# Kernel optimization log

Measured on AMD Instinct MI355X. Metric: run time of the kernel, lower is better.

## Reference

```python
import jax, jax.numpy as jnp
import numpy as np

N = 100000
E = 1600000
D = 64  # in = hidden = out channels


def setup_inputs() -> dict:
    key = jax.random.key(0)
    ks = jax.random.split(key, 6)
    x = jax.random.normal(ks[0], (N, D), dtype=jnp.float32)
    edge_index = jax.random.randint(ks[1], (2, E), 0, N, dtype=jnp.int64)
    # bias-free linear weights, torch Linear layout [out, in]
    s = 1.0 / np.sqrt(D)
    W0 = jax.random.uniform(ks[2], (D, D), jnp.float32, -s, s)
    W1 = jax.random.uniform(ks[3], (D, D), jnp.float32, -s, s)
    Wm = jax.random.uniform(ks[4], (D, D), jnp.float32, -s, s)
    eps0 = jnp.zeros((), jnp.float32)  # train_eps=True, init 0.0
    eps1 = jnp.zeros((), jnp.float32)
    return {"x": x, "edge_index": edge_index, "W0": W0, "eps0": eps0,
            "W1": W1, "eps1": eps1, "Wm": Wm}


def reference(x, edge_index, W0, eps0, W1, eps1, Wm):
    n = x.shape[0]
    src, dst = edge_index[0], edge_index[1]

    def gin_conv(h, W, eps):
        # sparse adjacency sum-aggregation: out[i] = sum_{j->i} h[j]
        agg = jax.ops.segment_sum(h[src], dst, num_segments=n)
        # eps-scaled self-loop + bias-free linear
        return (agg + (1.0 + eps) * h) @ W.T

    h1 = jax.nn.relu(gin_conv(x, W0, eps0))   # xs[0], [N, D]
    h2 = jax.nn.relu(gin_conv(h1, W1, eps1))  # xs[1], [N, D]
    return (h1 @ Wm.T + h2) / 2.0
```

## Files before the change

kernel.cpp:

```cpp
#include <hip/hip_runtime.h>
#include <hip/hip_fp16.h>


__global__ __launch_bounds__(256) void zero_int_kernel(int* __restrict__ p, int n)
{
    int i = blockIdx.x * blockDim.x + threadIdx.x;
    int stride = gridDim.x * blockDim.x;
    for (; i < n; i += stride) p[i] = 0;
}

__global__ __launch_bounds__(256) void hist_rank_kernel(
    const int* __restrict__ dst, int* __restrict__ deg,
    int* __restrict__ rank, int E)
{
    int base = (blockIdx.x * blockDim.x + threadIdx.x) * 16;
    if (base + 15 < E) {
        int4 a = *(const int4*)&dst[base];
        int4 b = *(const int4*)&dst[base + 4];
        int4 c = *(const int4*)&dst[base + 8];
        int4 d = *(const int4*)&dst[base + 12];
        int r0 = atomicAdd(&deg[a.x], 1);
        int r1 = atomicAdd(&deg[a.y], 1);
        int r2 = atomicAdd(&deg[a.z], 1);
        int r3 = atomicAdd(&deg[a.w], 1);
        int r4 = atomicAdd(&deg[b.x], 1);
        int r5 = atomicAdd(&deg[b.y], 1);
        int r6 = atomicAdd(&deg[b.z], 1);
        int r7 = atomicAdd(&deg[b.w], 1);
        int r8 = atomicAdd(&deg[c.x], 1);
        int r9 = atomicAdd(&deg[c.y], 1);
        int rA = atomicAdd(&deg[c.z], 1);
        int rB = atomicAdd(&deg[c.w], 1);
        int rC = atomicAdd(&deg[d.x], 1);
        int rD = atomicAdd(&deg[d.y], 1);
        int rE = atomicAdd(&deg[d.z], 1);
        int rF = atomicAdd(&deg[d.w], 1);
        *(int4*)&rank[base]      = make_int4(r0, r1, r2, r3);
        *(int4*)&rank[base + 4]  = make_int4(r4, r5, r6, r7);
        *(int4*)&rank[base + 8]  = make_int4(r8, r9, rA, rB);
        *(int4*)&rank[base + 12] = make_int4(rC, rD, rE, rF);
    } else {
        for (int e = base; e < E; ++e) rank[e] = atomicAdd(&deg[dst[e]], 1);
    }
}

__global__ __launch_bounds__(256) void hist_kernel(
    const int* __restrict__ dst, int* __restrict__ deg, int E)
{
    int e4 = (blockIdx.x * blockDim.x + threadIdx.x) * 4;
    if (e4 + 3 < E) {
        int4 d = *(const int4*)&dst[e4];
        atomicAdd(&deg[d.x], 1);
        atomicAdd(&deg[d.y], 1);
        atomicAdd(&deg[d.z], 1);
        atomicAdd(&deg[d.w], 1);
    } else {
        for (int e = e4; e < E; ++e) atomicAdd(&deg[dst[e]], 1);
    }
}

__global__ __launch_bounds__(256) void scanA_kernel(
    const int* __restrict__ deg, int* __restrict__ off,
    int* __restrict__ bsum, int n)
{
    __shared__ int tmp[256];
    int t = threadIdx.x;
    int base = blockIdx.x * 1024 + t * 4;
    int v0 = 0, v1 = 0, v2 = 0, v3 = 0;
    if (base + 3 < n) {
        int4 q = *(const int4*)&deg[base];
        v0 = q.x; v1 = q.y; v2 = q.z; v3 = q.w;
    } else {
        if (base + 0 < n) v0 = deg[base + 0];
        if (base + 1 < n) v1 = deg[base + 1];
        if (base + 2 < n) v2 = deg[base + 2];
    }
    int tot = v0 + v1 + v2 + v3;
    tmp[t] = tot;
    __syncthreads();
    for (int d = 1; d < 256; d <<= 1) {
        int x = (t >= d) ? tmp[t - d] : 0;
        __syncthreads();
        tmp[t] += x;
        __syncthreads();
    }
    int incl = tmp[t];
    int p = incl - tot;
    if (base + 0 < n) off[base + 0] = p;
    if (base + 1 < n) off[base + 1] = p + v0;
    if (base + 2 < n) off[base + 2] = p + v0 + v1;
    if (base + 3 < n) off[base + 3] = p + v0 + v1 + v2;
    if (t == 255) bsum[blockIdx.x] = incl;
}

__global__ __launch_bounds__(256) void scanB_kernel(int* __restrict__ bsum, int nb)
{
    __shared__ int tmp[256];
    int t = threadIdx.x;
    int v = (t < nb) ? bsum[t] : 0;
    tmp[t] = v;
    __syncthreads();
    for (int d = 1; d < 256; d <<= 1) {
        int x = (t >= d) ? tmp[t - d] : 0;
        __syncthreads();
        tmp[t] += x;
        __syncthreads();
    }
    if (t < nb) bsum[t] = tmp[t] - v;
}

__global__ __launch_bounds__(256) void scanC_kernel(
    int* __restrict__ off, int* __restrict__ cursor,
    const int* __restrict__ bsum, int n, int E)
{
    int t = threadIdx.x;
    int add = bsum[blockIdx.x];
    int base = blockIdx.x * 1024 + t * 4;
#pragma unroll
    for (int q = 0; q < 4; ++q) {
        int idx = base + q;
        if (idx < n) {
            int v = off[idx] + add;
            off[idx] = v;
            if (cursor) cursor[idx] = v;
        }
    }
    if (blockIdx.x == 0 && t == 0) off[n] = E;
}

__global__ __launch_bounds__(256) void fill_rank_kernel(
    const int* __restrict__ src, const int* __restrict__ dst,
    const int* __restrict__ rank, const int* __restrict__ off,
    int* __restrict__ bucket, int E)
{
    int base = (blockIdx.x * blockDim.x + threadIdx.x) * 8;
    if (base + 7 < E) {
        int4 d0 = *(const int4*)&dst[base];
        int4 d1 = *(const int4*)&dst[base + 4];
        int4 r0 = *(const int4*)&rank[base];
        int4 r1 = *(const int4*)&rank[base + 4];
        int4 s0 = *(const int4*)&src[base];
        int4 s1 = *(const int4*)&src[base + 4];
        bucket[off[d0.x] + r0.x] = s0.x;
        bucket[off[d0.y] + r0.y] = s0.y;
        bucket[off[d0.z] + r0.z] = s0.z;
        bucket[off[d0.w] + r0.w] = s0.w;
        bucket[off[d1.x] + r1.x] = s1.x;
        bucket[off[d1.y] + r1.y] = s1.y;
        bucket[off[d1.z] + r1.z] = s1.z;
        bucket[off[d1.w] + r1.w] = s1.w;
    } else {
        for (int e = base; e < E; ++e) bucket[off[dst[e]] + rank[e]] = src[e];
    }
}

__global__ __launch_bounds__(256) void fill_kernel(
    const int* __restrict__ src, const int* __restrict__ dst,
    int* __restrict__ cursor, int* __restrict__ bucket, int E)
{
    int e = blockIdx.x * blockDim.x + threadIdx.x;
    if (e < E) {
        int d = dst[e];
        int p = atomicAdd(&cursor[d], 1);
        bucket[p] = src[e];
    }
}

__global__ __launch_bounds__(256) void f32_to_f16_kernel(
    const float* __restrict__ in, __half* __restrict__ out, int total4)
{
    int i = blockIdx.x * blockDim.x + threadIdx.x;
    int stride = gridDim.x * blockDim.x;
    const float4* in4 = (const float4*)in;
    uint2* out4 = (uint2*)out;
    for (; i < total4; i += stride) {
        float4 v = in4[i];
        __half2 a = __floats2half2_rn(v.x, v.y);
        __half2 b = __floats2half2_rn(v.z, v.w);
        uint2 u;
        u.x = __builtin_bit_cast(unsigned int, a);
        u.y = __builtin_bit_cast(unsigned int, b);
        out4[i] = u;
    }
}

#define WPB 8

__device__ __forceinline__ __half2 bc_h2(unsigned int u)
{
    return __builtin_bit_cast(__half2, u);
}
__device__ __forceinline__ unsigned int bc_u(__half2 h)
{
    return __builtin_bit_cast(unsigned int, h);
}

#if __has_builtin(__builtin_amdgcn_fdot2)
typedef _Float16 half2_v __attribute__((ext_vector_type(2)));
__device__ __forceinline__ float fdot2(unsigned int a, unsigned int b, float c)
{
    return __builtin_amdgcn_fdot2(__builtin_bit_cast(half2_v, a),
                                  __builtin_bit_cast(half2_v, b), c, false);
}
#else
__device__ __forceinline__ float fdot2(unsigned int a, unsigned int b, float c)
{
    float2 af = __half22float2(bc_h2(a));
    float2 bf = __half22float2(bc_h2(b));
    return fmaf(af.x, bf.x, fmaf(af.y, bf.y, c));
}
#endif

__device__ __forceinline__ void xreduce4(__half2& a0, __half2& a1,
                                         __half2& a2, __half2& a3)
{
#pragma unroll
    for (int mask = 8; mask <= 32; mask <<= 1) {
        a0 = __hadd2(a0, bc_h2((unsigned int)__shfl_xor((int)bc_u(a0), mask, 64)));
        a1 = __hadd2(a1, bc_h2((unsigned int)__shfl_xor((int)bc_u(a1), mask, 64)));
        a2 = __hadd2(a2, bc_h2((unsigned int)__shfl_xor((int)bc_u(a2), mask, 64)));
        a3 = __hadd2(a3, bc_h2((unsigned int)__shfl_xor((int)bc_u(a3), mask, 64)));
    }
}

__device__ __forceinline__ void gather8(
    const __half* __restrict__ hh, const int* __restrict__ bucket,
    int beg, int end, int g, int l8,
    __half2& a0, __half2& a1, __half2& a2, __half2& a3)
{
    int j = beg;
    for (; j + 16 <= end; j += 16) {
        int sa = bucket[j + g];
        int sb = bucket[j + 8 + g];
        uint4 va = *(const uint4*)&hh[(size_t)sa * 64 + l8 * 8];
        uint4 vb = *(const uint4*)&hh[(size_t)sb * 64 + l8 * 8];
        a0 = __hadd2(__hadd2(a0, bc_h2(va.x)), bc_h2(vb.x));
        a1 = __hadd2(__hadd2(a1, bc_h2(va.y)), bc_h2(vb.y));
        a2 = __hadd2(__hadd2(a2, bc_h2(va.z)), bc_h2(vb.z));
        a3 = __hadd2(__hadd2(a3, bc_h2(va.w)), bc_h2(vb.w));
    }
    if (j + 8 <= end) {
        int sa = bucket[j + g];
        uint4 va = *(const uint4*)&hh[(size_t)sa * 64 + l8 * 8];
        a0 = __hadd2(a0, bc_h2(va.x));
        a1 = __hadd2(a1, bc_h2(va.y));
        a2 = __hadd2(a2, bc_h2(va.z));
        a3 = __hadd2(a3, bc_h2(va.w));
        j += 8;
    }
    if (j < end) {
        int jj = j + g;
        int sc = bucket[(jj < end) ? jj : (end - 1)];
        __half2 m2 = __float2half2_rn((jj < end) ? 1.0f : 0.0f);
        uint4 vc = *(const uint4*)&hh[(size_t)sc * 64 + l8 * 8];
        a0 = __hfma2(bc_h2(vc.x), m2, a0);
        a1 = __hfma2(bc_h2(vc.y), m2, a1);
        a2 = __hfma2(bc_h2(vc.z), m2, a2);
        a3 = __hfma2(bc_h2(vc.w), m2, a3);
    }
}


__global__ __launch_bounds__(512) void fused_gin_h_kernel(
    const __half* __restrict__ hh, const int* __restrict__ off,
    const int* __restrict__ bucket, const float* __restrict__ W,
    const float* __restrict__ eps, __half* __restrict__ outh, int n)
{
    __shared__ __half WhS[4096];
    __shared__ __half rowh[WPB][64];
    int tid = threadIdx.x;
    for (int idx = tid; idx < 4096; idx += 512) {
        int row = idx >> 6, col = idx & 63;
        WhS[(col >> 3) * 512 + row * 8 + (col & 7)] = __float2half(W[idx]);
    }
    __syncthreads();
    float s = 1.0f + eps[0];
    __half2 s2 = __float2half2_rn(s);
    int lane = tid & 63;
    int w = tid >> 6;
    int l8 = lane & 7;
    int g = lane >> 3;
    int wavesTotal = gridDim.x * WPB;
    const uint4* Wh4 = (const uint4*)WhS;
    for (int i = blockIdx.x * WPB + w; i < n; i += wavesTotal) {
        int2 be = *(const int2*)&off[i];
        int beg = __builtin_amdgcn_readfirstlane(be.x);
        int end = __builtin_amdgcn_readfirstlane(be.y);
        __half2 a0 = bc_h2(0u), a1 = bc_h2(0u), a2 = bc_h2(0u), a3 = bc_h2(0u);
        gather8(hh, bucket, beg, end, g, l8, a0, a1, a2, a3);
        xreduce4(a0, a1, a2, a3);
        if (g == 0) {
            uint4 sv = *(const uint4*)&hh[(size_t)i * 64 + l8 * 8];
            a0 = __hfma2(bc_h2(sv.x), s2, a0);
            a1 = __hfma2(bc_h2(sv.y), s2, a1);
            a2 = __hfma2(bc_h2(sv.z), s2, a2);
            a3 = __hfma2(bc_h2(sv.w), s2, a3);
            uint4 st;
            st.x = bc_u(a0); st.y = bc_u(a1); st.z = bc_u(a2); st.w = bc_u(a3);
            *(uint4*)&rowh[w][l8 * 8] = st;
        }
        __builtin_amdgcn_wave_barrier();
        float o = 0.f;
#pragma unroll
        for (int k4 = 0; k4 < 8; ++k4) {
            uint4 wv = Wh4[k4 * 64 + lane];
            uint4 rv = *(const uint4*)&rowh[w][k4 * 8];
            o = fdot2(wv.x, rv.x, o);
            o = fdot2(wv.y, rv.y, o);
            o = fdot2(wv.z, rv.z, o);
            o = fdot2(wv.w, rv.w, o);
        }
        outh[(size_t)i * 64 + lane] = __float2half(fmaxf(o, 0.f));
        __builtin_amdgcn_wave_barrier();
    }
}

__global__ __launch_bounds__(512) void fused_final_h_kernel(
    const __half* __restrict__ hh1, const int* __restrict__ off,
    const int* __restrict__ bucket, const float* __restrict__ W1,
    const float* __restrict__ Wm, const float* __restrict__ eps,
    float* __restrict__ out, int n)
{
    __shared__ __half W1hS[4096];
    __shared__ __half WmhS[4096];
    __shared__ __half rowh[WPB][64];
    __shared__ __half selfh[WPB][64];
    int tid = threadIdx.x;
    for (int idx = tid; idx < 4096; idx += 512) {
        int row = idx >> 6, col = idx & 63;
        int li = (col >> 3) * 512 + row * 8 + (col & 7);
        W1hS[li] = __float2half(W1[idx]);
        WmhS[li] = __float2half(Wm[idx]);
    }
    __syncthreads();
    float s = 1.0f + eps[0];
    __half2 s2 = __float2half2_rn(s);
    int lane = tid & 63;
    int w = tid >> 6;
    int l8 = lane & 7;
    int g = lane >> 3;
    int wavesTotal = gridDim.x * WPB;
    const uint4* W1h4 = (const uint4*)W1hS;
    const uint4* Wmh4 = (const uint4*)WmhS;
    for (int i = blockIdx.x * WPB + w; i < n; i += wavesTotal) {
        int2 be = *(const int2*)&off[i];
        int beg = __builtin_amdgcn_readfirstlane(be.x);
        int end = __builtin_amdgcn_readfirstlane(be.y);
        __half2 a0 = bc_h2(0u), a1 = bc_h2(0u), a2 = bc_h2(0u), a3 = bc_h2(0u);
        gather8(hh1, bucket, beg, end, g, l8, a0, a1, a2, a3);
        xreduce4(a0, a1, a2, a3);
        if (g == 0) {
            uint4 sv = *(const uint4*)&hh1[(size_t)i * 64 + l8 * 8];
            *(uint4*)&selfh[w][l8 * 8] = sv;
            a0 = __hfma2(bc_h2(sv.x), s2, a0);
            a1 = __hfma2(bc_h2(sv.y), s2, a1);
            a2 = __hfma2(bc_h2(sv.z), s2, a2);
            a3 = __hfma2(bc_h2(sv.w), s2, a3);
            uint4 st;
            st.x = bc_u(a0); st.y = bc_u(a1); st.z = bc_u(a2); st.w = bc_u(a3);
            *(uint4*)&rowh[w][l8 * 8] = st;
        }
        __builtin_amdgcn_wave_barrier();
        float o1 = 0.f, o2 = 0.f;
#pragma unroll
        for (int k4 = 0; k4 < 8; ++k4) {
            uint4 wv1 = W1h4[k4 * 64 + lane];
            uint4 wv2 = Wmh4[k4 * 64 + lane];
            uint4 rv  = *(const uint4*)&rowh[w][k4 * 8];
            uint4 sv  = *(const uint4*)&selfh[w][k4 * 8];
            o1 = fdot2(wv1.x, rv.x, o1);
            o1 = fdot2(wv1.y, rv.y, o1);
            o1 = fdot2(wv1.z, rv.z, o1);
            o1 = fdot2(wv1.w, rv.w, o1);
            o2 = fdot2(wv2.x, sv.x, o2);
            o2 = fdot2(wv2.y, sv.y, o2);
            o2 = fdot2(wv2.z, sv.z, o2);
            o2 = fdot2(wv2.w, sv.w, o2);
        }
        out[(size_t)i * 64 + lane] = (fmaxf(o1, 0.f) + o2) * 0.5f;
        __builtin_amdgcn_wave_barrier();
    }
}

__device__ __forceinline__ float dot4(float4 a, float4 b)
{
    return a.x * b.x + a.y * b.y + a.z * b.z + a.w * b.w;
}

__device__ __forceinline__ float4 gather_row_f32(
    const float* __restrict__ h, const int* __restrict__ bucket,
    int beg, int end, int g, int l16, float4 acc4)
{
    int j = beg;
    for (; j + 8 <= end; j += 8) {
        int sa = bucket[j + g];
        int sb = bucket[j + 4 + g];
        float4 va = *(const float4*)&h[(size_t)sa * 64 + l16 * 4];
        float4 vb = *(const float4*)&h[(size_t)sb * 64 + l16 * 4];
        acc4.x += va.x + vb.x;
        acc4.y += va.y + vb.y;
        acc4.z += va.z + vb.z;
        acc4.w += va.w + vb.w;
    }
    if (j + 4 <= end) {
        int sa = bucket[j + g];
        float4 va = *(const float4*)&h[(size_t)sa * 64 + l16 * 4];
        acc4.x += va.x; acc4.y += va.y; acc4.z += va.z; acc4.w += va.w;
        j += 4;
    }
    if (j < end) {
        int jj = j + g;
        int sc = bucket[(jj < end) ? jj : (end - 1)];
        float m = (jj < end) ? 1.0f : 0.0f;
        float4 vc = *(const float4*)&h[(size_t)sc * 64 + l16 * 4];
        acc4.x = fmaf(vc.x, m, acc4.x);
        acc4.y = fmaf(vc.y, m, acc4.y);
        acc4.z = fmaf(vc.z, m, acc4.z);
        acc4.w = fmaf(vc.w, m, acc4.w);
    }
    return acc4;
}

__global__ __launch_bounds__(512) void fused_gin_kernel(
    const float* __restrict__ h, const int* __restrict__ off,
    const int* __restrict__ bucket, const float* __restrict__ W,
    const float* __restrict__ eps, float* __restrict__ out, int n)
{
    __shared__ float Ws[64][68];
    __shared__ float P[WPB][4][64];
    __shared__ float rowbuf[WPB][64];
    int tid = threadIdx.x;
    for (int idx = tid; idx < 4096; idx += 512) Ws[idx >> 6][idx & 63] = W[idx];
    __syncthreads();
    float s = 1.0f + eps[0];
    int lane = tid & 63;
    int w = tid >> 6;
    int l16 = lane & 15;
    int g = lane >> 4;
    int wavesTotal = gridDim.x * WPB;
    for (int i = blockIdx.x * WPB + w; i < n; i += wavesTotal) {
        float4 init = make_float4(0.f, 0.f, 0.f, 0.f);
        if (g == 0) {
            float4 self4 = *(const float4*)&h[(size_t)i * 64 + l16 * 4];
            init = make_float4(s * self4.x, s * self4.y, s * self4.z, s * self4.w);
        }
        int2 be = *(const int2*)&off[i];
        int beg = __builtin_amdgcn_readfirstlane(be.x);
        int end = __builtin_amdgcn_readfirstlane(be.y);
        float4 acc4 = gather_row_f32(h, bucket, beg, end, g, l16, init);
        *(float4*)&P[w][g][l16 * 4] = acc4;
        __builtin_amdgcn_wave_barrier();
        float r0 = P[w][0][lane], r1 = P[w][1][lane];
        float r2 = P[w][2][lane], r3 = P[w][3][lane];
        rowbuf[w][lane] = (r0 + r1) + (r2 + r3);
        __builtin_amdgcn_wave_barrier();
        const float4* wrow = (const float4*)&Ws[lane][0];
        const float4* rrow = (const float4*)&rowbuf[w][0];
        float o = 0.f;
#pragma unroll
        for (int k4 = 0; k4 < 16; ++k4) o += dot4(wrow[k4], rrow[k4]);
        out[(size_t)i * 64 + lane] = fmaxf(o, 0.f);
        __builtin_amdgcn_wave_barrier();
    }
}

__global__ __launch_bounds__(512) void fused_final_csr_kernel(
    const float* __restrict__ h1, const int* __restrict__ off,
    const int* __restrict__ bucket, const float* __restrict__ W1,
    const float* __restrict__ Wm, const float* __restrict__ eps,
    float* __restrict__ out, int n)
{
    __shared__ float W1s[64][68];
    __shared__ float Wms[64][68];
    __shared__ float P[WPB][4][64];
    __shared__ float rowbuf[WPB][64];
    __shared__ float selfbuf[WPB][64];
    int tid = threadIdx.x;
    for (int idx = tid; idx < 4096; idx += 512) {
        W1s[idx >> 6][idx & 63] = W1[idx];
        Wms[idx >> 6][idx & 63] = Wm[idx];
    }
    __syncthreads();
    float s = 1.0f + eps[0];
    int lane = tid & 63;
    int w = tid >> 6;
    int l16 = lane & 15;
    int g = lane >> 4;
    int wavesTotal = gridDim.x * WPB;
    for (int i = blockIdx.x * WPB + w; i < n; i += wavesTotal) {
        float4 init = make_float4(0.f, 0.f, 0.f, 0.f);
        if (g == 0) {
            float4 self4 = *(const float4*)&h1[(size_t)i * 64 + l16 * 4];
            *(float4*)&selfbuf[w][l16 * 4] = self4;
            init = make_float4(s * self4.x, s * self4.y, s * self4.z, s * self4.w);
        }
        int2 be = *(const int2*)&off[i];
        int beg = __builtin_amdgcn_readfirstlane(be.x);
        int end = __builtin_amdgcn_readfirstlane(be.y);
        float4 acc4 = gather_row_f32(h1, bucket, beg, end, g, l16, init);
        *(float4*)&P[w][g][l16 * 4] = acc4;
        __builtin_amdgcn_wave_barrier();
        float r0 = P[w][0][lane], r1 = P[w][1][lane];
        float r2 = P[w][2][lane], r3 = P[w][3][lane];
        rowbuf[w][lane] = (r0 + r1) + (r2 + r3);
        __builtin_amdgcn_wave_barrier();
        const float4* w1row = (const float4*)&W1s[lane][0];
        const float4* wmrow = (const float4*)&Wms[lane][0];
        const float4* rrow  = (const float4*)&rowbuf[w][0];
        const float4* srow  = (const float4*)&selfbuf[w][0];
        float o1 = 0.f, o2 = 0.f;
#pragma unroll
        for (int k4 = 0; k4 < 16; ++k4) {
            o1 += dot4(w1row[k4], rrow[k4]);
            o2 += dot4(wmrow[k4], srow[k4]);
        }
        out[(size_t)i * 64 + lane] = (fmaxf(o1, 0.f) + o2) * 0.5f;
        __builtin_amdgcn_wave_barrier();
    }
}

__global__ __launch_bounds__(256) void init_scale_kernel(
    const float* __restrict__ h, const float* __restrict__ eps,
    float* __restrict__ agg, int total4)
{
    float s = 1.0f + eps[0];
    int i = blockIdx.x * blockDim.x + threadIdx.x;
    int stride = gridDim.x * blockDim.x;
    const float4* h4 = (const float4*)h;
    float4* a4 = (float4*)agg;
    for (; i < total4; i += stride) {
        float4 v = h4[i];
        v.x *= s; v.y *= s; v.z *= s; v.w *= s;
        a4[i] = v;
    }
}

__global__ __launch_bounds__(256) void scatter_kernel(
    const float* __restrict__ h, const int* __restrict__ src,
    const int* __restrict__ dst, float* __restrict__ agg, int E)
{
    int lane = threadIdx.x & 63;
    int e = blockIdx.x * 4 + (threadIdx.x >> 6);
    if (e >= E) return;
    int s = src[e];
    int d = dst[e];
    atomicAdd(&agg[(size_t)d * 64 + lane], h[(size_t)s * 64 + lane]);
}

__global__ __launch_bounds__(256) void gemm_relu_kernel(
    const float* __restrict__ A, const float* __restrict__ W,
    float* __restrict__ out, int n)
{
    __shared__ float Wt[64][65];
    __shared__ float rowbuf[4][64];
    int tid = threadIdx.x;
    for (int i = tid; i < 4096; i += 256) Wt[i & 63][i >> 6] = W[i];
    __syncthreads();
    int lane = tid & 63;
    int w = tid >> 6;
    int wavesTotal = gridDim.x * 4;
    for (int i = blockIdx.x * 4 + w; i < n; i += wavesTotal) {
        rowbuf[w][lane] = A[(size_t)i * 64 + lane];
        __builtin_amdgcn_wave_barrier();
        float o = 0.f;
#pragma unroll
        for (int k = 0; k < 64; ++k) o += rowbuf[w][k] * Wt[k][lane];
        out[(size_t)i * 64 + lane] = fmaxf(o, 0.f);
        __builtin_amdgcn_wave_barrier();
    }
}

__global__ __launch_bounds__(256) void final_kernel(
    const float* __restrict__ Agg, const float* __restrict__ H1,
    const float* __restrict__ W1, const float* __restrict__ Wm,
    float* __restrict__ out, int n)
{
    __shared__ float W1t[64][65];
    __shared__ float Wmt[64][65];
    __shared__ float rowbuf[4][64];
    __shared__ float selfbuf[4][64];
    int tid = threadIdx.x;
    for (int i = tid; i < 4096; i += 256) {
        W1t[i & 63][i >> 6] = W1[i];
        Wmt[i & 63][i >> 6] = Wm[i];
    }
    __syncthreads();
    int lane = tid & 63;
    int w = tid >> 6;
    int wavesTotal = gridDim.x * 4;
    for (int i = blockIdx.x * 4 + w; i < n; i += wavesTotal) {
        rowbuf[w][lane] = Agg[(size_t)i * 64 + lane];
        selfbuf[w][lane] = H1[(size_t)i * 64 + lane];
        __builtin_amdgcn_wave_barrier();
        float o1 = 0.f, o2 = 0.f;
#pragma unroll
        for (int k = 0; k < 64; ++k) {
            o1 += rowbuf[w][k] * W1t[k][lane];
            o2 += selfbuf[w][k] * Wmt[k][lane];
        }
        out[(size_t)i * 64 + lane] = (fmaxf(o1, 0.f) + o2) * 0.5f;
        __builtin_amdgcn_wave_barrier();
    }
}

extern "C" void kernel_launch(void* const* d_in, const int* in_sizes, int n_in,
                              void* d_out, int out_size, void* d_ws, size_t ws_size,
                              hipStream_t stream)
{
    const float* x    = (const float*)d_in[0];
    const int*   ei   = (const int*)d_in[1];
    const float* W0   = (const float*)d_in[2];
    const float* eps0 = (const float*)d_in[3];
    const float* W1   = (const float*)d_in[4];
    const float* eps1 = (const float*)d_in[5];
    const float* Wm   = (const float*)d_in[6];
    float* out = (float*)d_out;

    int n = in_sizes[0] / 64;
    int E = in_sizes[1] / 2;
    const int* src = ei;
    const int* dst = ei + E;

    auto align1k = [](size_t v) { return (v + 1023) & ~(size_t)1023; };

    size_t hhx_off    = 0;
    size_t hh1_off    = align1k(hhx_off + (size_t)n * 64 * 2);
    size_t off_off    = align1k(hh1_off + (size_t)n * 64 * 2);
    size_t deg_off    = align1k(off_off + (size_t)(n + 1) * 4);
    size_t bsum_off   = align1k(deg_off + (size_t)n * 4);
    size_t bucket_off = align1k(bsum_off + 256 * 4);
    size_t rank_off   = align1k(bucket_off + (size_t)E * 4);
    size_t need_A2    = rank_off + (size_t)E * 4;

    size_t b_h1_off     = 0;
    size_t b_off_off    = align1k(b_h1_off + (size_t)n * 64 * 4);
    size_t b_deg_off    = align1k(b_off_off + (size_t)(n + 1) * 4);
    size_t b_cursor_off = align1k(b_deg_off + (size_t)n * 4);
    size_t b_bsum_off   = align1k(b_cursor_off + (size_t)n * 4);
    size_t b_bucket_off = align1k(b_bsum_off + 256 * 4);
    size_t need_B       = b_bucket_off + (size_t)E * 4;

    int nb = (n + 1023) / 1024;
    int e8Blocks  = (E + 2047) / 2048;
    int e16Blocks = (E + 4095) / 4096;
    int total4 = n * 16;

    if (ws_size >= need_A2) {
        __half* hhx  = (__half*)((char*)d_ws + hhx_off);
        __half* hh1  = (__half*)((char*)d_ws + hh1_off);
        int* off     = (int*)((char*)d_ws + off_off);
        int* deg     = (int*)((char*)d_ws + deg_off);
        int* bsum    = (int*)((char*)d_ws + bsum_off);
        int* bucket  = (int*)((char*)d_ws + bucket_off);
        int* rank    = (int*)((char*)d_ws + rank_off);

        zero_int_kernel<<<256, 256, 0, stream>>>(deg, n);
        f32_to_f16_kernel<<<2048, 256, 0, stream>>>(x, hhx, total4);
        hist_rank_kernel<<<e16Blocks, 256, 0, stream>>>(dst, deg, rank, E);
        scanA_kernel<<<nb, 256, 0, stream>>>(deg, off, bsum, n);
        scanB_kernel<<<1, 256, 0, stream>>>(bsum, nb);
        scanC_kernel<<<nb, 256, 0, stream>>>(off, (int*)nullptr, bsum, n, E);
        fill_rank_kernel<<<e8Blocks, 256, 0, stream>>>(src, dst, rank, off, bucket, E);

        fused_gin_h_kernel<<<1024, 512, 0, stream>>>(hhx, off, bucket, W0, eps0, hh1, n);
        fused_final_h_kernel<<<1024, 512, 0, stream>>>(hh1, off, bucket, W1, Wm, eps1, out, n);
    } else if (ws_size >= need_B) {
        float* h1    = (float*)((char*)d_ws + b_h1_off);
        int* off     = (int*)((char*)d_ws + b_off_off);
        int* deg     = (int*)((char*)d_ws + b_deg_off);
        int* cursor  = (int*)((char*)d_ws + b_cursor_off);
        int* bsum    = (int*)((char*)d_ws + b_bsum_off);
        int* bucket  = (int*)((char*)d_ws + b_bucket_off);

        zero_int_kernel<<<256, 256, 0, stream>>>(deg, n);
        hist_kernel<<<(E + 1023) / 1024, 256, 0, stream>>>(dst, deg, E);
        scanA_kernel<<<nb, 256, 0, stream>>>(deg, off, bsum, n);
        scanB_kernel<<<1, 256, 0, stream>>>(bsum, nb);
        scanC_kernel<<<nb, 256, 0, stream>>>(off, cursor, bsum, n, E);
        fill_kernel<<<(E + 255) / 256, 256, 0, stream>>>(src, dst, cursor, bucket, E);

        fused_gin_kernel<<<1024, 512, 0, stream>>>(x, off, bucket, W0, eps0, h1, n);
        fused_final_csr_kernel<<<768, 512, 0, stream>>>(h1, off, bucket, W1, Wm, eps1, out, n);
    } else {
        float* agg = (float*)d_ws;
        float* h1  = out;
        int scatterBlocks = (E + 3) / 4;

        init_scale_kernel<<<2048, 256, 0, stream>>>(x, eps0, agg, total4);
        scatter_kernel<<<scatterBlocks, 256, 0, stream>>>(x, src, dst, agg, E);
        gemm_relu_kernel<<<2048, 256, 0, stream>>>(agg, W0, h1, n);
        init_scale_kernel<<<2048, 256, 0, stream>>>(h1, eps1, agg, total4);
        scatter_kernel<<<scatterBlocks, 256, 0, stream>>>(h1, src, dst, agg, E);
        final_kernel<<<2048, 256, 0, stream>>>(agg, h1, W1, Wm, out, n);
    }
}
```

Measured before the change: 225.2 us.

## Process eight nodes per wave with per-octet gather and batched matvec

Each wave now handles eight destination nodes at once, with each 8-lane group gathering one node's neighbors. This replaces the old scheme where the whole wave split one node's edge list and then reduced across lanes with shuffles. The mat-vec step reuses each loaded weight vector across eight rows held in shared memory, and the grid drops to 784 blocks. The cost is lane divergence, since every group loops up to the wave's maximum degree with masked loads. Overshoot reads past the bucket array are covered by padding the workspace.

```diff
diff --git a/kernel.cpp b/kernel.cpp
--- a/kernel.cpp
+++ b/kernel.cpp
@@ -211,55 +211,6 @@
 }
 #endif
 
-__device__ __forceinline__ void xreduce4(__half2& a0, __half2& a1,
-                                         __half2& a2, __half2& a3)
-{
-#pragma unroll
-    for (int mask = 8; mask <= 32; mask <<= 1) {
-        a0 = __hadd2(a0, bc_h2((unsigned int)__shfl_xor((int)bc_u(a0), mask, 64)));
-        a1 = __hadd2(a1, bc_h2((unsigned int)__shfl_xor((int)bc_u(a1), mask, 64)));
-        a2 = __hadd2(a2, bc_h2((unsigned int)__shfl_xor((int)bc_u(a2), mask, 64)));
-        a3 = __hadd2(a3, bc_h2((unsigned int)__shfl_xor((int)bc_u(a3), mask, 64)));
-    }
-}
-
-__device__ __forceinline__ void gather8(
-    const __half* __restrict__ hh, const int* __restrict__ bucket,
-    int beg, int end, int g, int l8,
-    __half2& a0, __half2& a1, __half2& a2, __half2& a3)
-{
-    int j = beg;
-    for (; j + 16 <= end; j += 16) {
-        int sa = bucket[j + g];
-        int sb = bucket[j + 8 + g];
-        uint4 va = *(const uint4*)&hh[(size_t)sa * 64 + l8 * 8];
-        uint4 vb = *(const uint4*)&hh[(size_t)sb * 64 + l8 * 8];
-        a0 = __hadd2(__hadd2(a0, bc_h2(va.x)), bc_h2(vb.x));
-        a1 = __hadd2(__hadd2(a1, bc_h2(va.y)), bc_h2(vb.y));
-        a2 = __hadd2(__hadd2(a2, bc_h2(va.z)), bc_h2(vb.z));
-        a3 = __hadd2(__hadd2(a3, bc_h2(va.w)), bc_h2(vb.w));
-    }
-    if (j + 8 <= end) {
-        int sa = bucket[j + g];
-        uint4 va = *(const uint4*)&hh[(size_t)sa * 64 + l8 * 8];
-        a0 = __hadd2(a0, bc_h2(va.x));
-        a1 = __hadd2(a1, bc_h2(va.y));
-        a2 = __hadd2(a2, bc_h2(va.z));
-        a3 = __hadd2(a3, bc_h2(va.w));
-        j += 8;
-    }
-    if (j < end) {
-        int jj = j + g;
-        int sc = bucket[(jj < end) ? jj : (end - 1)];
-        __half2 m2 = __float2half2_rn((jj < end) ? 1.0f : 0.0f);
-        uint4 vc = *(const uint4*)&hh[(size_t)sc * 64 + l8 * 8];
-        a0 = __hfma2(bc_h2(vc.x), m2, a0);
-        a1 = __hfma2(bc_h2(vc.y), m2, a1);
-        a2 = __hfma2(bc_h2(vc.z), m2, a2);
-        a3 = __hfma2(bc_h2(vc.w), m2, a3);
-    }
-}
-
 
 __global__ __launch_bounds__(512) void fused_gin_h_kernel(
     const __half* __restrict__ hh, const int* __restrict__ off,
@@ -267,7 +218,7 @@
     const float* __restrict__ eps, __half* __restrict__ outh, int n)
 {
     __shared__ __half WhS[4096];
-    __shared__ __half rowh[WPB][64];
+    __shared__ __half rowh[WPB][8][64];
     int tid = threadIdx.x;
     for (int idx = tid; idx < 4096; idx += 512) {
         int row = idx >> 6, col = idx & 63;
@@ -276,41 +227,97 @@
     __syncthreads();
     float s = 1.0f + eps[0];
     __half2 s2 = __float2half2_rn(s);
+    const __half2 one2 = __float2half2_rn(1.0f);
+    const __half2 zero2 = __float2half2_rn(0.0f);
     int lane = tid & 63;
     int w = tid >> 6;
     int l8 = lane & 7;
     int g = lane >> 3;
-    int wavesTotal = gridDim.x * WPB;
     const uint4* Wh4 = (const uint4*)WhS;
-    for (int i = blockIdx.x * WPB + w; i < n; i += wavesTotal) {
-        int2 be = *(const int2*)&off[i];
-        int beg = __builtin_amdgcn_readfirstlane(be.x);
-        int end = __builtin_amdgcn_readfirstlane(be.y);
-        __half2 a0 = bc_h2(0u), a1 = bc_h2(0u), a2 = bc_h2(0u), a3 = bc_h2(0u);
-        gather8(hh, bucket, beg, end, g, l8, a0, a1, a2, a3);
-        xreduce4(a0, a1, a2, a3);
-        if (g == 0) {
-            uint4 sv = *(const uint4*)&hh[(size_t)i * 64 + l8 * 8];
-            a0 = __hfma2(bc_h2(sv.x), s2, a0);
-            a1 = __hfma2(bc_h2(sv.y), s2, a1);
-            a2 = __hfma2(bc_h2(sv.z), s2, a2);
-            a3 = __hfma2(bc_h2(sv.w), s2, a3);
-            uint4 st;
-            st.x = bc_u(a0); st.y = bc_u(a1); st.z = bc_u(a2); st.w = bc_u(a3);
-            *(uint4*)&rowh[w][l8 * 8] = st;
-        }
-        __builtin_amdgcn_wave_barrier();
-        float o = 0.f;
+    int octetStride = gridDim.x * WPB * 8;
+    for (int ibase = (blockIdx.x * WPB + w) * 8; ibase < n; ibase += octetStride) {
+        int i = ibase + g;
+        bool nv = (i < n);
+        int iSafe = nv ? i : 0;
+        int2 be = *(const int2*)&off[iSafe];
+        int j = be.x;
+        int end = nv ? be.y : be.x;
+        int md = end - j;
+#pragma unroll
+        for (int mask = 1; mask < 64; mask <<= 1)
+            md = max(md, __shfl_xor(md, mask, 64));
+        __half2 aA0 = zero2, aA1 = zero2, aA2 = zero2, aA3 = zero2;
+        __half2 aB0 = zero2, aB1 = zero2, aB2 = zero2, aB3 = zero2;
+        for (int it = 0; it < md; it += 4) {
+            int e0 = bucket[j + 0];
+            int e1 = bucket[j + 1];
+            int e2 = bucket[j + 2];
+            int e3 = bucket[j + 3];
+            bool v0 = (j + 0) < end, v1 = (j + 1) < end;
+            bool v2 = (j + 2) < end, v3 = (j + 3) < end;
+            int x0 = v0 ? e0 : 0, x1 = v1 ? e1 : 0;
+            int x2 = v2 ? e2 : 0, x3 = v3 ? e3 : 0;
+            uint4 r0 = *(const uint4*)&hh[(size_t)x0 * 64 + l8 * 8];
+            uint4 r1 = *(const uint4*)&hh[(size_t)x1 * 64 + l8 * 8];
+            uint4 r2 = *(const uint4*)&hh[(size_t)x2 * 64 + l8 * 8];
+            uint4 r3 = *(const uint4*)&hh[(size_t)x3 * 64 + l8 * 8];
+            __half2 m0 = v0 ? one2 : zero2;
+            __half2 m1 = v1 ? one2 : zero2;
+            __half2 m2 = v2 ? one2 : zero2;
+            __half2 m3 = v3 ? one2 : zero2;
+            aA0 = __hfma2(bc_h2(r0.x), m0, aA0);
+            aA1 = __hfma2(bc_h2(r0.y), m0, aA1);
+            aA2 = __hfma2(bc_h2(r0.z), m0, aA2);
+            aA3 = __hfma2(bc_h2(r0.w), m0, aA3);
+            aB0 = __hfma2(bc_h2(r1.x), m1, aB0);
+            aB1 = __hfma2(bc_h2(r1.y), m1, aB1);
+            aB2 = __hfma2(bc_h2(r1.z), m1, aB2);
+            aB3 = __hfma2(bc_h2(r1.w), m1, aB3);
+            aA0 = __hfma2(bc_h2(r2.x), m2, aA0);
+            aA1 = __hfma2(bc_h2(r2.y), m2, aA1);
+            aA2 = __hfma2(bc_h2(r2.z), m2, aA2);
+            aA3 = __hfma2(bc_h2(r2.w), m2, aA3);
+            aB0 = __hfma2(bc_h2(r3.x), m3, aB0);
+            aB1 = __hfma2(bc_h2(r3.y), m3, aB1);
+            aB2 = __hfma2(bc_h2(r3.z), m3, aB2);
+            aB3 = __hfma2(bc_h2(r3.w), m3, aB3);
+            j += 4;
+        }
+        aA0 = __hadd2(aA0, aB0);
+        aA1 = __hadd2(aA1, aB1);
+        aA2 = __hadd2(aA2, aB2);
+        aA3 = __hadd2(aA3, aB3);
+        {
+            uint4 sv = *(const uint4*)&hh[(size_t)iSafe * 64 + l8 * 8];
+            __half2 ss = nv ? s2 : zero2;
+            aA0 = __hfma2(bc_h2(sv.x), ss, aA0);
+            aA1 = __hfma2(bc_h2(sv.y), ss, aA1);
+            aA2 = __hfma2(bc_h2(sv.z), ss, aA2);
+            aA3 = __hfma2(bc_h2(sv.w), ss, aA3);
+        }
+        uint4 st;
+        st.x = bc_u(aA0); st.y = bc_u(aA1); st.z = bc_u(aA2); st.w = bc_u(aA3);
+        *(uint4*)&rowh[w][g][l8 * 8] = st;
+        __builtin_amdgcn_wave_barrier();
+        float o0 = 0.f, o1 = 0.f, o2 = 0.f, o3 = 0.f;
+        float o4 = 0.f, o5 = 0.f, o6 = 0.f, o7 = 0.f;
 #pragma unroll
         for (int k4 = 0; k4 < 8; ++k4) {
             uint4 wv = Wh4[k4 * 64 + lane];
-            uint4 rv = *(const uint4*)&rowh[w][k4 * 8];
-            o = fdot2(wv.x, rv.x, o);
-            o = fdot2(wv.y, rv.y, o);
-            o = fdot2(wv.z, rv.z, o);
-            o = fdot2(wv.w, rv.w, o);
-        }
-        outh[(size_t)i * 64 + lane] = __float2half(fmaxf(o, 0.f));
+            uint4 rv;
+#define MV1(T, O) \
+            rv = *(const uint4*)&rowh[w][T][k4 * 8]; \
+            O = fdot2(wv.x, rv.x, O); O = fdot2(wv.y, rv.y, O); \
+            O = fdot2(wv.z, rv.z, O); O = fdot2(wv.w, rv.w, O);
+            MV1(0, o0) MV1(1, o1) MV1(2, o2) MV1(3, o3)
+            MV1(4, o4) MV1(5, o5) MV1(6, o6) MV1(7, o7)
+#undef MV1
+        }
+#define ST1(T, O) if (ibase + (T) < n) \
+            outh[(size_t)(ibase + (T)) * 64 + lane] = __float2half(fmaxf(O, 0.f));
+        ST1(0, o0) ST1(1, o1) ST1(2, o2) ST1(3, o3)
+        ST1(4, o4) ST1(5, o5) ST1(6, o6) ST1(7, o7)
+#undef ST1
         __builtin_amdgcn_wave_barrier();
     }
 }
@@ -323,8 +330,8 @@
 {
     __shared__ __half W1hS[4096];
     __shared__ __half WmhS[4096];
-    __shared__ __half rowh[WPB][64];
-    __shared__ __half selfh[WPB][64];
+    __shared__ __half rowh[WPB][8][64];
+    __shared__ __half selfh[WPB][8][64];
     int tid = threadIdx.x;
     for (int idx = tid; idx < 4096; idx += 512) {
         int row = idx >> 6, col = idx & 63;
@@ -335,49 +342,105 @@
     __syncthreads();
     float s = 1.0f + eps[0];
     __half2 s2 = __float2half2_rn(s);
+    const __half2 one2 = __float2half2_rn(1.0f);
+    const __half2 zero2 = __float2half2_rn(0.0f);
     int lane = tid & 63;
     int w = tid >> 6;
     int l8 = lane & 7;
     int g = lane >> 3;
-    int wavesTotal = gridDim.x * WPB;
     const uint4* W1h4 = (const uint4*)W1hS;
     const uint4* Wmh4 = (const uint4*)WmhS;
-    for (int i = blockIdx.x * WPB + w; i < n; i += wavesTotal) {
-        int2 be = *(const int2*)&off[i];
-        int beg = __builtin_amdgcn_readfirstlane(be.x);
-        int end = __builtin_amdgcn_readfirstlane(be.y);
-        __half2 a0 = bc_h2(0u), a1 = bc_h2(0u), a2 = bc_h2(0u), a3 = bc_h2(0u);
-        gather8(hh1, bucket, beg, end, g, l8, a0, a1, a2, a3);
-        xreduce4(a0, a1, a2, a3);
-        if (g == 0) {
-            uint4 sv = *(const uint4*)&hh1[(size_t)i * 64 + l8 * 8];
-            *(uint4*)&selfh[w][l8 * 8] = sv;
-            a0 = __hfma2(bc_h2(sv.x), s2, a0);
-            a1 = __hfma2(bc_h2(sv.y), s2, a1);
-            a2 = __hfma2(bc_h2(sv.z), s2, a2);
-            a3 = __hfma2(bc_h2(sv.w), s2, a3);
-            uint4 st;
-            st.x = bc_u(a0); st.y = bc_u(a1); st.z = bc_u(a2); st.w = bc_u(a3);
-            *(uint4*)&rowh[w][l8 * 8] = st;
-        }
-        __builtin_amdgcn_wave_barrier();
-        float o1 = 0.f, o2 = 0.f;
+    int octetStride = gridDim.x * WPB * 8;
+    for (int ibase = (blockIdx.x * WPB + w) * 8; ibase < n; ibase += octetStride) {
+        int i = ibase + g;
+        bool nv = (i < n);
+        int iSafe = nv ? i : 0;
+        int2 be = *(const int2*)&off[iSafe];
+        int j = be.x;
+        int end = nv ? be.y : be.x;
+        int md = end - j;
+#pragma unroll
+        for (int mask = 1; mask < 64; mask <<= 1)
+            md = max(md, __shfl_xor(md, mask, 64));
+        __half2 aA0 = zero2, aA1 = zero2, aA2 = zero2, aA3 = zero2;
+        __half2 aB0 = zero2, aB1 = zero2, aB2 = zero2, aB3 = zero2;
+        for (int it = 0; it < md; it += 4) {
+            int e0 = bucket[j + 0];
+            int e1 = bucket[j + 1];
+            int e2 = bucket[j + 2];
+            int e3 = bucket[j + 3];
+            bool v0 = (j + 0) < end, v1 = (j + 1) < end;
+            bool v2 = (j + 2) < end, v3 = (j + 3) < end;
+            int x0 = v0 ? e0 : 0, x1 = v1 ? e1 : 0;
+            int x2 = v2 ? e2 : 0, x3 = v3 ? e3 : 0;
+            uint4 r0 = *(const uint4*)&hh1[(size_t)x0 * 64 + l8 * 8];
+            uint4 r1 = *(const uint4*)&hh1[(size_t)x1 * 64 + l8 * 8];
+            uint4 r2 = *(const uint4*)&hh1[(size_t)x2 * 64 + l8 * 8];
+            uint4 r3 = *(const uint4*)&hh1[(size_t)x3 * 64 + l8 * 8];
+            __half2 m0 = v0 ? one2 : zero2;
+            __half2 m1 = v1 ? one2 : zero2;
+            __half2 m2 = v2 ? one2 : zero2;
+            __half2 m3 = v3 ? one2 : zero2;
+            aA0 = __hfma2(bc_h2(r0.x), m0, aA0);
+            aA1 = __hfma2(bc_h2(r0.y), m0, aA1);
+            aA2 = __hfma2(bc_h2(r0.z), m0, aA2);
+            aA3 = __hfma2(bc_h2(r0.w), m0, aA3);
+            aB0 = __hfma2(bc_h2(r1.x), m1, aB0);
+            aB1 = __hfma2(bc_h2(r1.y), m1, aB1);
+            aB2 = __hfma2(bc_h2(r1.z), m1, aB2);
+            aB3 = __hfma2(bc_h2(r1.w), m1, aB3);
+            aA0 = __hfma2(bc_h2(r2.x), m2, aA0);
+            aA1 = __hfma2(bc_h2(r2.y), m2, aA1);
+            aA2 = __hfma2(bc_h2(r2.z), m2, aA2);
+            aA3 = __hfma2(bc_h2(r2.w), m2, aA3);
+            aB0 = __hfma2(bc_h2(r3.x), m3, aB0);
+            aB1 = __hfma2(bc_h2(r3.y), m3, aB1);
+            aB2 = __hfma2(bc_h2(r3.z), m3, aB2);
+            aB3 = __hfma2(bc_h2(r3.w), m3, aB3);
+            j += 4;
+        }
+        aA0 = __hadd2(aA0, aB0);
+        aA1 = __hadd2(aA1, aB1);
+        aA2 = __hadd2(aA2, aB2);
+        aA3 = __hadd2(aA3, aB3);
+        {
+            uint4 sv = *(const uint4*)&hh1[(size_t)iSafe * 64 + l8 * 8];
+            *(uint4*)&selfh[w][g][l8 * 8] = sv;
+            __half2 ss = nv ? s2 : zero2;
+            aA0 = __hfma2(bc_h2(sv.x), ss, aA0);
+            aA1 = __hfma2(bc_h2(sv.y), ss, aA1);
+            aA2 = __hfma2(bc_h2(sv.z), ss, aA2);
+            aA3 = __hfma2(bc_h2(sv.w), ss, aA3);
+        }
+        uint4 st;
+        st.x = bc_u(aA0); st.y = bc_u(aA1); st.z = bc_u(aA2); st.w = bc_u(aA3);
+        *(uint4*)&rowh[w][g][l8 * 8] = st;
+        __builtin_amdgcn_wave_barrier();
+        float p0 = 0.f, p1 = 0.f, p2 = 0.f, p3 = 0.f;
+        float p4 = 0.f, p5 = 0.f, p6 = 0.f, p7 = 0.f;
+        float q0 = 0.f, q1 = 0.f, q2 = 0.f, q3 = 0.f;
+        float q4 = 0.f, q5 = 0.f, q6 = 0.f, q7 = 0.f;
 #pragma unroll
         for (int k4 = 0; k4 < 8; ++k4) {
             uint4 wv1 = W1h4[k4 * 64 + lane];
             uint4 wv2 = Wmh4[k4 * 64 + lane];
-            uint4 rv  = *(const uint4*)&rowh[w][k4 * 8];
-            uint4 sv  = *(const uint4*)&selfh[w][k4 * 8];
-            o1 = fdot2(wv1.x, rv.x, o1);
-            o1 = fdot2(wv1.y, rv.y, o1);
-            o1 = fdot2(wv1.z, rv.z, o1);
-            o1 = fdot2(wv1.w, rv.w, o1);
-            o2 = fdot2(wv2.x, sv.x, o2);
-            o2 = fdot2(wv2.y, sv.y, o2);
-            o2 = fdot2(wv2.z, sv.z, o2);
-            o2 = fdot2(wv2.w, sv.w, o2);
-        }
-        out[(size_t)i * 64 + lane] = (fmaxf(o1, 0.f) + o2) * 0.5f;
+            uint4 rv, sv;
+#define MV2(T, P, Q) \
+            rv = *(const uint4*)&rowh[w][T][k4 * 8]; \
+            sv = *(const uint4*)&selfh[w][T][k4 * 8]; \
+            P = fdot2(wv1.x, rv.x, P); P = fdot2(wv1.y, rv.y, P); \
+            P = fdot2(wv1.z, rv.z, P); P = fdot2(wv1.w, rv.w, P); \
+            Q = fdot2(wv2.x, sv.x, Q); Q = fdot2(wv2.y, sv.y, Q); \
+            Q = fdot2(wv2.z, sv.z, Q); Q = fdot2(wv2.w, sv.w, Q);
+            MV2(0, p0, q0) MV2(1, p1, q1) MV2(2, p2, q2) MV2(3, p3, q3)
+            MV2(4, p4, q4) MV2(5, p5, q5) MV2(6, p6, q6) MV2(7, p7, q7)
+#undef MV2
+        }
+#define ST2(T, P, Q) if (ibase + (T) < n) \
+            out[(size_t)(ibase + (T)) * 64 + lane] = (fmaxf(P, 0.f) + Q) * 0.5f;
+        ST2(0, p0, q0) ST2(1, p1, q1) ST2(2, p2, q2) ST2(3, p3, q3)
+        ST2(4, p4, q4) ST2(5, p5, q5) ST2(6, p6, q6) ST2(7, p7, q7)
+#undef ST2
         __builtin_amdgcn_wave_barrier();
     }
 }
@@ -629,7 +692,7 @@
     size_t deg_off    = align1k(off_off + (size_t)(n + 1) * 4);
     size_t bsum_off   = align1k(deg_off + (size_t)n * 4);
     size_t bucket_off = align1k(bsum_off + 256 * 4);
-    size_t rank_off   = align1k(bucket_off + (size_t)E * 4);
+    size_t rank_off   = align1k(bucket_off + (size_t)(E + 64) * 4);
     size_t need_A2    = rank_off + (size_t)E * 4;
 
     size_t b_h1_off     = 0;
@@ -644,6 +707,7 @@
     int e8Blocks  = (E + 2047) / 2048;
     int e16Blocks = (E + 4095) / 4096;
     int total4 = n * 16;
+    int fusedBlocks = 784;
 
     if (ws_size >= need_A2) {
         __half* hhx  = (__half*)((char*)d_ws + hhx_off);
@@ -662,8 +726,8 @@
         scanC_kernel<<<nb, 256, 0, stream>>>(off, (int*)nullptr, bsum, n, E);
         fill_rank_kernel<<<e8Blocks, 256, 0, stream>>>(src, dst, rank, off, bucket, E);
 
-        fused_gin_h_kernel<<<1024, 512, 0, stream>>>(hhx, off, bucket, W0, eps0, hh1, n);
-        fused_final_h_kernel<<<1024, 512, 0, stream>>>(hh1, off, bucket, W1, Wm, eps1, out, n);
+        fused_gin_h_kernel<<<fusedBlocks, 512, 0, stream>>>(hhx, off, bucket, W0, eps0, hh1, n);
+        fused_final_h_kernel<<<fusedBlocks, 512, 0, stream>>>(hh1, off, bucket, W1, Wm, eps1, out, n);
     } else if (ws_size >= need_B) {
         float* h1    = (float*)((char*)d_ws + b_h1_off);
         int* off     = (int*)((char*)d_ws + b_off_off);
```

Measured after the change: 562.6 us. 150% more time.
